# Kernel tuning notes

Hardware: AMD Instinct MI355X
Metric: run time of the kernel (lower is better)

Reference implementation:

```python
import jax, jax.numpy as jnp
import numpy as np

N = 4096; E = 32768; H = 128; R = 32; L = 2
CUT_UP = 5.0; MAX_Z = 100

def cosine_cutoff(d):
    c = 0.5 * (jnp.cos(d * (np.pi / CUT_UP)) + 1.0)
    return c * (d < CUT_UP).astype(d.dtype)

def tensor_norm(t):
    return (t * t).sum((-2, -1))

def decompose_tensor(t):
    eye = jnp.eye(3, dtype=t.dtype)
    I = (jnp.trace(t, axis1=-2, axis2=-1) / 3.0)[..., None, None] * eye
    tT = jnp.swapaxes(t, -2, -1)
    A = 0.5 * (t - tT)
    S = 0.5 * (t + tT) - I
    return I, A, S

def vector_to_skewtensor(v):
    x, y, z = v[..., 0], v[..., 1], v[..., 2]
    o = jnp.zeros_like(x)
    return jnp.stack([o, -z, y, z, o, -x, -y, x, o], axis=-1).reshape(v.shape[:-1] + (3, 3))

def vector_to_symtensor(v):
    t = v[..., :, None] * v[..., None, :]
    eye = jnp.eye(3, dtype=v.dtype)
    I = (jnp.trace(t, axis1=-2, axis2=-1) / 3.0)[..., None, None] * eye
    return t - I  # symmetric already, 0.5*(t+t^T) == t

def cmix(T, W):  # nn.Linear(H,H,bias=False) over the channel dim of [N,H,3,3]
    return jnp.einsum('nhij,hk->nkij', T, W)

def layernorm(x, g, b, eps=1e-5):
    m = x.mean(-1, keepdims=True)
    v = ((x - m) ** 2).mean(-1, keepdims=True)
    return (x - m) / jnp.sqrt(v + eps) * g + b

def setup_inputs():
    key = jax.random.key(0)
    ks = iter(jax.random.split(key, 48))
    def nrm(shape, fan_in):
        return jax.random.normal(next(ks), shape, jnp.float32) / np.sqrt(fan_in)
    inp = {}
    inp['z'] = jax.random.randint(next(ks), (N,), 0, MAX_Z)
    inp['edge_index'] = jax.random.randint(next(ks), (2, E), 0, N)
    inp['edge_weight'] = jax.random.uniform(next(ks), (E,), jnp.float32) * CUT_UP
    inp['edge_vec'] = jax.random.normal(next(ks), (E, 3), jnp.float32)
    inp['edge_attr'] = jax.random.normal(next(ks), (E, R), jnp.float32)
    inp['emb_table'] = nrm((MAX_Z, H), H)
    inp['dp1_w'] = nrm((R, H), R); inp['dp1_b'] = jnp.zeros((H,))
    inp['dp2_w'] = nrm((R, H), R); inp['dp2_b'] = jnp.zeros((H,))
    inp['dp3_w'] = nrm((R, H), R); inp['dp3_b'] = jnp.zeros((H,))
    inp['emb2_w'] = nrm((2 * H, H), 2 * H); inp['emb2_b'] = jnp.zeros((H,))
    inp['tne_lt'] = nrm((3, H, H), H)
    inp['tne_s0_w'] = nrm((H, 2 * H), H); inp['tne_s0_b'] = jnp.zeros((2 * H,))
    inp['tne_s1_w'] = nrm((2 * H, 3 * H), 2 * H); inp['tne_s1_b'] = jnp.zeros((3 * H,))
    inp['ln_g'] = jnp.ones((H,)); inp['ln_b'] = jnp.zeros((H,))
    inp['msg_l0_w'] = nrm((L, R, H), R); inp['msg_l0_b'] = jnp.zeros((L, H))
    inp['msg_l1_w'] = nrm((L, H, 2 * H), H); inp['msg_l1_b'] = jnp.zeros((L, 2 * H))
    inp['msg_l2_w'] = nrm((L, 2 * H, 3 * H), 2 * H); inp['msg_l2_b'] = jnp.zeros((L, 3 * H))
    inp['msg_lx'] = nrm((L, 3, H, H), H)
    inp['msg_lt'] = nrm((L, 3, H, H), H)
    return inp

def _forward(z, edge_index, edge_weight, edge_vec, edge_attr, emb_table,
             dp1_w, dp1_b, dp2_w, dp2_b, dp3_w, dp3_b, emb2_w, emb2_b,
             tne_lt, tne_s0_w, tne_s0_b, tne_s1_w, tne_s1_b, ln_g, ln_b,
             msg_l0_w, msg_l0_b, msg_l1_w, msg_l1_b, msg_l2_w, msg_l2_b,
             msg_lx, msg_lt):
    src, dst = edge_index[0], edge_index[1]
    eye = jnp.eye(3, dtype=jnp.float32)
    segsum = lambda x: jax.ops.segment_sum(x, dst, num_segments=N)
    silu = jax.nn.silu
    # ---- TensorNeighborEmbedding ----
    Z = emb_table[z]                                     # [N,H]
    C = cosine_cutoff(edge_weight)                       # [E]
    W1 = (edge_attr @ dp1_w + dp1_b) * C[:, None]
    W2 = (edge_attr @ dp2_w + dp2_b) * C[:, None]
    W3 = (edge_attr @ dp3_w + dp3_b) * C[:, None]
    mask = (src != dst)[:, None]
    vn = jnp.linalg.norm(edge_vec, axis=-1, keepdims=True)
    ev = jnp.where(mask, edge_vec / jnp.maximum(vn, 1e-12), edge_vec)
    skew = vector_to_skewtensor(ev)                      # [E,3,3]
    sym = vector_to_symtensor(ev)                        # [E,3,3]
    Zij = jnp.concatenate([Z[dst], Z[src]], axis=-1) @ emb2_w + emb2_b  # [E,H]
    # I channel is a scaled identity per edge -> factor the eye out of the scatter
    In = segsum(Zij * W1)[..., None, None] * eye                         # [N,H,3,3]
    An = segsum((Zij * W2)[:, :, None, None] * skew[:, None])            # [N,H,3,3]
    Sn = segsum((Zij * W3)[:, :, None, None] * sym[:, None])             # [N,H,3,3]
    norm = layernorm(tensor_norm(In + An + Sn), ln_g, ln_b)              # [N,H]
    In = cmix(In, tne_lt[0]); An = cmix(An, tne_lt[1]); Sn = cmix(Sn, tne_lt[2])
    fsc = silu(silu(norm @ tne_s0_w + tne_s0_b) @ tne_s1_w + tne_s1_b).reshape(N, H, 3)
    X = (fsc[..., 0, None, None] * In + fsc[..., 1, None, None] * An
         + fsc[..., 2, None, None] * Sn)
    # ---- TensorMessage layers ----
    for l in range(L):
        ea = silu(edge_attr @ msg_l0_w[l] + msg_l0_b[l])
        ea = silu(ea @ msg_l1_w[l] + msg_l1_b[l])
        ea = silu(ea @ msg_l2_w[l] + msg_l2_b[l])
        ea = (ea * C[:, None]).reshape(E, H, 3)
        X = X / (tensor_norm(X) + 1.0)[..., None, None]
        I, A, S = decompose_tensor(X)
        I = cmix(I, msg_lx[l, 0]); A = cmix(A, msg_lx[l, 1]); S = cmix(S, msg_lx[l, 2])
        Y = I + A + S
        Im = segsum(ea[:, :, 0, None, None] * I[src])    # gather -> scale -> scatter
        Am = segsum(ea[:, :, 1, None, None] * A[src])
        Sm = segsum(ea[:, :, 2, None, None] * S[src])
        msg = Im + Am + Sm
        AB = msg @ Y + Y @ msg                           # batched 3x3 matmuls
        I, A, S = decompose_tensor(AB)
        d = (tensor_norm(I + A + S) + 1.0)[..., None, None]
        I = cmix(I / d, msg_lt[l, 0]); A = cmix(A / d, msg_lt[l, 1]); S = cmix(S / d, msg_lt[l, 2])
        dX = I + A + S
        dX = dX + dX @ dX
        X = X + dX
    return X

def reference(z, edge_index, edge_weight, edge_vec, edge_attr, emb_table,
              dp1_w, dp1_b, dp2_w, dp2_b, dp3_w, dp3_b, emb2_w, emb2_b,
              tne_lt, tne_s0_w, tne_s0_b, tne_s1_w, tne_s1_b, ln_g, ln_b,
              msg_l0_w, msg_l0_b, msg_l1_w, msg_l1_b, msg_l2_w, msg_l2_b,
              msg_lx, msg_lt):
    return _forward(z, edge_index, edge_weight, edge_vec, edge_attr, emb_table,
                    dp1_w, dp1_b, dp2_w, dp2_b, dp3_w, dp3_b, emb2_w, emb2_b,
                    tne_lt, tne_s0_w, tne_s0_b, tne_s1_w, tne_s1_b, ln_g, ln_b,
                    msg_l0_w, msg_l0_b, msg_l1_w, msg_l1_b, msg_l2_w, msg_l2_b,
                    msg_lx, msg_lt)
```

## Files before the change

kernel.cpp:

```cpp
#include <hip/hip_runtime.h>
#include <hip/hip_bf16.h>

typedef __hip_bfloat16 bf16;
typedef __attribute__((ext_vector_type(8))) short short8v;
typedef __attribute__((ext_vector_type(4))) float f32x4;

#define NN 4096
#define NE 32768
#define HH 128
#define MAXZ 100
#define TPB 8
#define NB 2


__device__ __forceinline__ float b2f(bf16 v){ return __bfloat162float(v); }
__device__ __forceinline__ float ldf(const float* p, size_t i){ return p[i]; }
__device__ __forceinline__ float ldf(const bf16*  p, size_t i){ return __bfloat162float(p[i]); }
__device__ __forceinline__ float siluf(float x){ return x / (1.0f + __expf(-x)); }
__device__ __forceinline__ unsigned short f2bu(float x){
  bf16 h = __float2bfloat16(x);
  return *reinterpret_cast<unsigned short*>(&h);
}
__device__ __forceinline__ float bround(float x){
  bf16 h = __float2bfloat16(x);
  return __bfloat162float(h);
}

__global__ void __launch_bounds__(256) k_detect(const unsigned int* __restrict__ w, int* __restrict__ flag){
  __shared__ int cnt[256];
  int t = threadIdx.x;
  int c = 0;
  for (int i = t; i < 4096; i += 256){
    unsigned int lo = w[i] & 0xffffu;
    int e = (int)((lo >> 7) & 0xffu);
    c += (e >= 110 && e <= 132) ? 1 : 0;
  }
  cnt[t] = c; __syncthreads();
  for (int off=128; off>=1; off>>=1){ if (t<off) cnt[t]+=cnt[t+off]; __syncthreads(); }
  if (t==0) flag[0] = (cnt[0] < 2048) ? 1 : 0;
}

__global__ void __launch_bounds__(256) k_count(const int* __restrict__ dst, int* __restrict__ counts){
  int e = blockIdx.x*256 + threadIdx.x;
  if (e < NE) atomicAdd(&counts[dst[e]], 1);
}

__global__ void __launch_bounds__(1024) k_scan(const int* __restrict__ counts, int* __restrict__ offsets, int* __restrict__ cursor){
  __shared__ int lds[1024];
  int t = threadIdx.x;
  int c0 = counts[4*t+0], c1 = counts[4*t+1], c2 = counts[4*t+2], c3 = counts[4*t+3];
  int s1 = c0+c1, s2 = s1+c2, s3 = s2+c3;
  lds[t] = s3;
  __syncthreads();
  for (int off=1; off<1024; off<<=1){
    int v = lds[t];
    int add = (t>=off)? lds[t-off] : 0;
    __syncthreads();
    lds[t] = v + add;
    __syncthreads();
  }
  int incl = lds[t];
  int base = incl - s3;
  offsets[4*t+0]=base;    offsets[4*t+1]=base+c0; offsets[4*t+2]=base+s1; offsets[4*t+3]=base+s2;
  cursor [4*t+0]=base;    cursor [4*t+1]=base+c0; cursor [4*t+2]=base+s1; cursor [4*t+3]=base+s2;
  if (t==1023) offsets[4096]=incl;
}

__global__ void __launch_bounds__(256) k_fill(const int* __restrict__ dst, const int* __restrict__ src,
                                              int* __restrict__ cursor,
                                              int* __restrict__ pos, int* __restrict__ csrc){
  int e = blockIdx.x*256 + threadIdx.x;
  if (e < NE){
    int p = atomicAdd(&cursor[dst[e]], 1);
    pos[e] = p;
    csrc[p] = src[e];
  }
}

template<typename T>
__device__ __forceinline__ void geom_impl(const T* ew, const T* evec,
    const int* src, const int* dst, const int* pos, float* gC, float* gVp){
  int e = blockIdx.x*256 + threadIdx.x;
  if (e >= NE) return;
  float d = ldf(ew, e);
  float c = 0.5f*(cosf(d*0.6283185307179586f)+1.0f);
  c = (d < 5.0f) ? c : 0.0f;
  gC[e] = c;
  float x = ldf(evec, (size_t)e*3+0), y = ldf(evec, (size_t)e*3+1), z = ldf(evec, (size_t)e*3+2);
  if (src[e] != dst[e]){
    float n = sqrtf(x*x+y*y+z*z);
    float inv = 1.0f/fmaxf(n, 1e-12f);
    x*=inv; y*=inv; z*=inv;
  }
  int p = pos[e];
  gVp[p*3+0]=x; gVp[p*3+1]=y; gVp[p*3+2]=z;
}
__global__ void __launch_bounds__(256) k_geom(const void* ew, const void* evec,
    const int* __restrict__ src, const int* __restrict__ dst, const int* __restrict__ pos,
    float* __restrict__ gC, float* __restrict__ gVp, const int* __restrict__ flag){
  if (flag[0]) geom_impl<float>((const float*)ew, (const float*)evec, src, dst, pos, gC, gVp);
  else         geom_impl<bf16 >((const bf16* )ew, (const bf16* )evec, src, dst, pos, gC, gVp);
}

template<typename T>
__device__ __forceinline__ void zemb_impl(const T* emb, const T* emb2_w,
    float* P1z, float* P2z, float* Zr){
  int zv = blockIdx.x, h = threadIdx.x;
  Zr[h] = ldf(emb, (size_t)zv*HH + h);
  __syncthreads();
  float p1=0.f, p2=0.f;
  for (int r=0;r<128;++r){
    float x = Zr[r];
    p1 += x*ldf(emb2_w, (size_t)r*HH+h);
    p2 += x*ldf(emb2_w, (size_t)(r+128)*HH+h);
  }
  P1z[zv*HH+h]=p1; P2z[zv*HH+h]=p2;
}
__global__ void __launch_bounds__(128) k_zemb(const void* emb, const void* emb2_w,
    float* __restrict__ P1z, float* __restrict__ P2z, const int* __restrict__ flag){
  __shared__ float Zr[128];
  if (flag[0]) zemb_impl<float>((const float*)emb, (const float*)emb2_w, P1z, P2z, Zr);
  else         zemb_impl<bf16 >((const bf16* )emb, (const bf16* )emb2_w, P1z, P2z, Zr);
}

__global__ void __launch_bounds__(256) k_cvt_attr(const void* in, unsigned short* __restrict__ out,
                                                  const int* __restrict__ flag){
  int i = blockIdx.x*256 + threadIdx.x;
  if (flag[0]) out[i] = f2bu(((const float*)in)[i]);
  else         out[i] = ((const unsigned short*)in)[i];
}

struct PackDescs {
  const void*     base[23];
  long            eoff[23];
  unsigned short* out[23];
  int K[23]; int N[23];
};
template<typename T>
__device__ __forceinline__ void pack_impl(const PackDescs& d){
  int y = blockIdx.y;
  int K = d.K[y], N = d.N[y];
  int ktiles = K>>5, ntiles = N>>4;
  int total = ktiles*ntiles*64;
  int idx = blockIdx.x*256 + threadIdx.x;
  if (idx >= total) return;
  int lane = idx & 63, tile = idx >> 6;
  int kt = tile % ktiles, nt = tile / ktiles;
  const T* W = (const T*)d.base[y] + d.eoff[y];
  int n = nt*16 + (lane&15), k0 = kt*32 + (lane>>4)*8;
  unsigned int t[8];
  #pragma unroll
  for (int j=0;j<8;++j) t[j] = f2bu(ldf(W, (size_t)(k0+j)*N + n));
  uint4 v;
  v.x = t[0] | (t[1]<<16);
  v.y = t[2] | (t[3]<<16);
  v.z = t[4] | (t[5]<<16);
  v.w = t[6] | (t[7]<<16);
  *reinterpret_cast<uint4*>(d.out[y] + ((size_t)tile*64 + lane)*8) = v;
}
__global__ void __launch_bounds__(256) k_pack(PackDescs d, const int* __restrict__ flag){
  if (flag[0]) pack_impl<float>(d);
  else         pack_impl<bf16 >(d);
}

template<typename T>
__device__ __forceinline__ void tne_edge_impl(
  const T* eattr, const int* src, const int* dst, const int* z, const int* pos,
  const T* dp1_w, const T* dp1_b, const T* dp2_w, const T* dp2_b,
  const T* dp3_w, const T* dp3_b, const T* emb2_b,
  const float* P1z, const float* P2z, const float* gC, bf16* eabuf,
  float (*attr)[32], int* zd, int* zs, int* ppos)
{
  int e0 = blockIdx.x*TPB;
  int h  = threadIdx.x;
  for (int i=h; i<TPB*32; i+=128) attr[i>>5][i&31] = ldf(eattr, (size_t)e0*32 + i);
  if (h < TPB){ int e=e0+h; zd[h]=z[dst[e]]; zs[h]=z[src[e]]; ppos[h]=pos[e]; }
  __syncthreads();
  float w1[TPB], w2[TPB], w3[TPB];
  float b1v=ldf(dp1_b,h), b2v=ldf(dp2_b,h), b3v=ldf(dp3_b,h);
  #pragma unroll
  for (int e=0;e<TPB;++e){ w1[e]=b1v; w2[e]=b2v; w3[e]=b3v; }
  for (int r=0;r<32;++r){
    float u1=ldf(dp1_w,(size_t)r*HH+h), u2=ldf(dp2_w,(size_t)r*HH+h), u3=ldf(dp3_w,(size_t)r*HH+h);
    #pragma unroll
    for (int e=0;e<TPB;++e){ float a=attr[e][r]; w1[e]+=a*u1; w2[e]+=a*u2; w3[e]+=a*u3; }
  }
  float eb = ldf(emb2_b,h);
  #pragma unroll
  for (int e=0;e<TPB;++e){
    float zij = P1z[zd[e]*HH+h] + P2z[zs[e]*HH+h] + eb;
    float c = gC[e0+e];
    bf16* p = eabuf + (size_t)ppos[e]*384;
    p[h]     = __float2bfloat16(zij*w1[e]*c);
    p[128+h] = __float2bfloat16(zij*w2[e]*c);
    p[256+h] = __float2bfloat16(zij*w3[e]*c);
  }
}
__global__ void __launch_bounds__(128) k_tne_edge(
  const void* eattr, const int* __restrict__ src, const int* __restrict__ dst,
  const int* __restrict__ z, const int* __restrict__ pos,
  const void* dp1_w, const void* dp1_b, const void* dp2_w, const void* dp2_b,
  const void* dp3_w, const void* dp3_b, const void* emb2_b,
  const float* __restrict__ P1z, const float* __restrict__ P2z,
  const float* __restrict__ gC, bf16* __restrict__ eabuf, const int* __restrict__ flag)
{
  __shared__ float attr[TPB][32];
  __shared__ int zd[TPB], zs[TPB], ppos[TPB];
  if (flag[0]) tne_edge_impl<float>((const float*)eattr, src, dst, z, pos,
      (const float*)dp1_w, (const float*)dp1_b, (const float*)dp2_w, (const float*)dp2_b,
      (const float*)dp3_w, (const float*)dp3_b, (const float*)emb2_b, P1z, P2z, gC, eabuf, attr, zd, zs, ppos);
  else tne_edge_impl<bf16>((const bf16*)eattr, src, dst, z, pos,
      (const bf16*)dp1_w, (const bf16*)dp1_b, (const bf16*)dp2_w, (const bf16*)dp2_b,
      (const bf16*)dp3_w, (const bf16*)dp3_b, (const bf16*)emb2_b, P1z, P2z, gC, eabuf, attr, zd, zs, ppos);
}

template<typename T>
__device__ __forceinline__ void tne_scat_impl(
  const int* offsets, const float* gVp, const bf16* eabuf,
  const T* ln_g, const T* ln_b, bf16* sm10, bf16* lnO, float* red)
{
  int n0 = blockIdx.x*NB, h = threadIdx.x;
  float tnv[NB];
  #pragma unroll
  for (int nn=0;nn<NB;++nn){
    int n = n0+nn;
    float a=0, v0=0,v1=0,v2=0, s0=0,s1=0,s2=0,s3=0,s4=0,s5=0;
    int beg = offsets[n], end = offsets[n+1];
    int i = beg;
    for (; i+4 <= end; i += 4){
      float c1[4],c2[4],c3[4],vx[4],vy[4],vz[4];
      #pragma unroll
      for (int u=0;u<4;++u){
        const bf16* p = eabuf + (size_t)(i+u)*384;
        c1[u]=b2f(p[h]); c2[u]=b2f(p[128+h]); c3[u]=b2f(p[256+h]);
        vx[u]=gVp[(i+u)*3+0]; vy[u]=gVp[(i+u)*3+1]; vz[u]=gVp[(i+u)*3+2];
      }
      #pragma unroll
      for (int u=0;u<4;++u){
        float tr3 = (vx[u]*vx[u]+vy[u]*vy[u]+vz[u]*vz[u])*(1.0f/3.0f);
        a  += c1[u];
        v0 += c2[u]*vx[u]; v1 += c2[u]*vy[u]; v2 += c2[u]*vz[u];
        s0 += c3[u]*(vx[u]*vx[u] - tr3); s1 += c3[u]*vx[u]*vy[u]; s2 += c3[u]*vx[u]*vz[u];
        s3 += c3[u]*(vy[u]*vy[u] - tr3); s4 += c3[u]*vy[u]*vz[u]; s5 += c3[u]*(vz[u]*vz[u] - tr3);
      }
    }
    for (; i<end; ++i){
      const bf16* p = eabuf + (size_t)i*384;
      float c1 = b2f(p[h]), c2 = b2f(p[128+h]), c3 = b2f(p[256+h]);
      float vx = gVp[i*3+0], vy = gVp[i*3+1], vz = gVp[i*3+2];
      float tr3 = (vx*vx+vy*vy+vz*vz)*(1.0f/3.0f);
      a  += c1;
      v0 += c2*vx; v1 += c2*vy; v2 += c2*vz;
      s0 += c3*(vx*vx - tr3); s1 += c3*vx*vy;          s2 += c3*vx*vz;
      s3 += c3*(vy*vy - tr3); s4 += c3*vy*vz;          s5 += c3*(vz*vz - tr3);
    }
    bf16* sp = sm10 + (size_t)n*1280;
    sp[0*128+h]=__float2bfloat16(a);
    sp[1*128+h]=__float2bfloat16(v0); sp[2*128+h]=__float2bfloat16(v1); sp[3*128+h]=__float2bfloat16(v2);
    sp[4*128+h]=__float2bfloat16(s0); sp[5*128+h]=__float2bfloat16(s1); sp[6*128+h]=__float2bfloat16(s2);
    sp[7*128+h]=__float2bfloat16(s3); sp[8*128+h]=__float2bfloat16(s4); sp[9*128+h]=__float2bfloat16(s5);
    tnv[nn] = 3.0f*a*a + 2.0f*(v0*v0+v1*v1+v2*v2)
            + s0*s0 + s3*s3 + s5*s5 + 2.0f*(s1*s1 + s2*s2 + s4*s4);
  }
  float gg = ldf(ln_g,h), bb = ldf(ln_b,h);
  #pragma unroll
  for (int nn=0;nn<NB;++nn){
    __syncthreads();
    red[h] = tnv[nn]; __syncthreads();
    for (int off=64; off>=1; off>>=1){ if (h<off) red[h]+=red[h+off]; __syncthreads(); }
    float mean = red[0]*(1.0f/128.0f);
    __syncthreads();
    float dm = tnv[nn] - mean;
    red[h] = dm*dm; __syncthreads();
    for (int off=64; off>=1; off>>=1){ if (h<off) red[h]+=red[h+off]; __syncthreads(); }
    float var = red[0]*(1.0f/128.0f);
    lnO[(size_t)(n0+nn)*128 + h] = __float2bfloat16(dm*rsqrtf(var+1e-5f)*gg + bb);
  }
}
__global__ void __launch_bounds__(128) k_tne_scat(
  const int* __restrict__ offsets, const float* __restrict__ gVp, const bf16* __restrict__ eabuf,
  const void* ln_g, const void* ln_b, bf16* __restrict__ sm10, bf16* __restrict__ lnO,
  const int* __restrict__ flag)
{
  __shared__ float red[128];
  if (flag[0]) tne_scat_impl<float>(offsets, gVp, eabuf, (const float*)ln_g, (const float*)ln_b, sm10, lnO, red);
  else         tne_scat_impl<bf16 >(offsets, gVp, eabuf, (const bf16* )ln_g, (const bf16* )ln_b, sm10, lnO, red);
}

template<typename T>
__device__ __forceinline__ void node_mlp_impl(
  const bf16* lnO, const unsigned short* ps0, const unsigned short* ps1,
  const T* b0, const T* b1, bf16* fsc3, unsigned short* h2p)
{
  int wid  = threadIdx.x >> 6;
  int lane = threadIdx.x & 63;
  int n0 = blockIdx.x*16;
  int m = lane & 15, g = lane >> 4;
  short8v aln[4];
  #pragma unroll
  for (int ks=0; ks<4; ++ks)
    aln[ks] = *reinterpret_cast<const short8v*>((const unsigned short*)lnO + (size_t)(n0+m)*128 + ks*32 + g*8);
  for (int nt=wid; nt<16; nt+=4){
    float bias = ldf(b0, nt*16+m);
    f32x4 acc = {bias,bias,bias,bias};
    #pragma unroll
    for (int ks=0; ks<4; ++ks){
      short8v b = *reinterpret_cast<const short8v*>(ps0 + ((size_t)(nt*4+ks)*64 + lane)*8);
      acc = __builtin_amdgcn_mfma_f32_16x16x32_bf16(aln[ks], b, acc, 0,0,0);
    }
    #pragma unroll
    for (int r=0;r<4;++r){
      int n = nt*16 + m, row = g*4 + r;
      h2p[(n>>5)*512 + (((n>>3)&3)*16+row)*8 + (n&7)] = f2bu(siluf(acc[r]));
    }
  }
  __syncthreads();
  short8v a3[8];
  #pragma unroll
  for (int ks=0; ks<8; ++ks) a3[ks] = *reinterpret_cast<const short8v*>(&h2p[ks*512 + lane*8]);
  for (int nt=wid; nt<24; nt+=4){
    float bias = ldf(b1, nt*16+m);
    f32x4 acc = {bias,bias,bias,bias};
    #pragma unroll
    for (int ks=0; ks<8; ++ks){
      short8v b = *reinterpret_cast<const short8v*>(ps1 + ((size_t)(nt*8+ks)*64 + lane)*8);
      acc = __builtin_amdgcn_mfma_f32_16x16x32_bf16(a3[ks], b, acc, 0,0,0);
    }
    #pragma unroll
    for (int r=0;r<4;++r){
      int n = nt*16 + m, row = g*4 + r;
      ((unsigned short*)fsc3)[(size_t)(n0+row)*384 + (n%3)*128 + (n/3)] = f2bu(siluf(acc[r]));
    }
  }
}
__global__ void __launch_bounds__(256) k_node_mlp(
  const bf16* __restrict__ lnO, const unsigned short* __restrict__ ps0,
  const unsigned short* __restrict__ ps1,
  const void* b0, const void* b1, bf16* __restrict__ fsc3, const int* __restrict__ flag)
{
  __shared__ __align__(16) unsigned short h2p[4096];
  if (flag[0]) node_mlp_impl<float>(lnO, ps0, ps1, (const float*)b0, (const float*)b1, fsc3, h2p);
  else         node_mlp_impl<bf16 >(lnO, ps0, ps1, (const bf16* )b0, (const bf16* )b1, fsc3, h2p);
}

__global__ void __launch_bounds__(256) k_tne_cmix(
  const bf16* __restrict__ sm10, const unsigned short* __restrict__ pwlt,
  const bf16* __restrict__ fsc3, float* __restrict__ X9)
{
  int wid  = threadIdx.x >> 6;
  int lane = threadIdx.x & 63;
  int n0 = blockIdx.x*16;
  int m = lane & 15, g = lane >> 4;
  f32x4 acc[10][2];
  #pragma unroll
  for (int c=0;c<10;++c){ acc[c][0]=(f32x4){0,0,0,0}; acc[c][1]=(f32x4){0,0,0,0}; }
  #pragma unroll
  for (int c=0;c<10;++c){
    int mat = (c==0) ? 0 : (c<4) ? 1 : 2;
    const unsigned short* bw = pwlt + (size_t)mat*16384;
    short8v af[4];
    #pragma unroll
    for (int ks=0; ks<4; ++ks)
      af[ks] = *reinterpret_cast<const short8v*>((const unsigned short*)sm10 + (size_t)(n0+m)*1280 + c*128 + ks*32 + g*8);
    #pragma unroll
    for (int t=0;t<2;++t){
      int nt = wid + t*4;
      #pragma unroll
      for (int ks=0; ks<4; ++ks){
        short8v b = *reinterpret_cast<const short8v*>(bw + ((size_t)(nt*4+ks)*64 + lane)*8);
        acc[c][t] = __builtin_amdgcn_mfma_f32_16x16x32_bf16(af[ks], b, acc[c][t], 0,0,0);
      }
    }
  }
  #pragma unroll
  for (int t=0;t<2;++t){
    int nt = wid + t*4;
    int h = nt*16 + m;
    #pragma unroll
    for (int r=0;r<4;++r){
      int node = n0 + g*4 + r;
      float am  = acc[0][t][r];
      float wm0 = acc[1][t][r], wm1 = acc[2][t][r], wm2 = acc[3][t][r];
      float t0 = acc[4][t][r], t1 = acc[5][t][r], t2 = acc[6][t][r];
      float t3 = acc[7][t][r], t4 = acc[8][t][r], t5 = acc[9][t][r];
      float f0 = b2f(fsc3[(size_t)node*384 + h]);
      float f1 = b2f(fsc3[(size_t)node*384 + 128 + h]);
      float f2 = b2f(fsc3[(size_t)node*384 + 256 + h]);
      float* xp = X9 + (size_t)node*1152;
      xp[0*128+h] = f0*am + f2*t0;
      xp[1*128+h] = -f1*wm2 + f2*t1;
      xp[2*128+h] =  f1*wm1 + f2*t2;
      xp[3*128+h] =  f1*wm2 + f2*t1;
      xp[4*128+h] = f0*am + f2*t3;
      xp[5*128+h] = -f1*wm0 + f2*t4;
      xp[6*128+h] = -f1*wm1 + f2*t2;
      xp[7*128+h] =  f1*wm0 + f2*t4;
      xp[8*128+h] = f0*am + f2*t5;
    }
  }
}

__global__ void __launch_bounds__(256) k_cmix_norm(
  float* __restrict__ X9, const unsigned short* __restrict__ pw, bf16* __restrict__ Y10)
{
  __shared__ __align__(16) unsigned short sst[16*1280];
  int n0 = blockIdx.x*16;
  int tid = threadIdx.x;
  #pragma unroll
  for (int it=0; it<8; ++it){
    int idx = it*256 + tid;
    int nn = idx >> 7, h = idx & 127;
    float* xp = X9 + (size_t)(n0+nn)*1152;
    float x00=xp[0*128+h], x01=xp[1*128+h], x02=xp[2*128+h];
    float x10=xp[3*128+h], x11=xp[4*128+h], x12=xp[5*128+h];
    float x20=xp[6*128+h], x21=xp[7*128+h], x22=xp[8*128+h];
    float tn = x00*x00+x01*x01+x02*x02+x10*x10+x11*x11+x12*x12+x20*x20+x21*x21+x22*x22;
    float inv = 1.0f/(tn+1.0f);
    x00*=inv; x01*=inv; x02*=inv; x10*=inv; x11*=inv; x12*=inv; x20*=inv; x21*=inv; x22*=inv;
    xp[0*128+h]=x00; xp[1*128+h]=x01; xp[2*128+h]=x02;
    xp[3*128+h]=x10; xp[4*128+h]=x11; xp[5*128+h]=x12;
    xp[6*128+h]=x20; xp[7*128+h]=x21; xp[8*128+h]=x22;
    float a = (x00+x11+x22)*(1.0f/3.0f);
    unsigned short* sp = sst + (size_t)nn*1280;
    sp[0*128+h]=f2bu(a);
    sp[1*128+h]=f2bu(0.5f*(x21-x12));
    sp[2*128+h]=f2bu(0.5f*(x02-x20));
    sp[3*128+h]=f2bu(0.5f*(x10-x01));
    sp[4*128+h]=f2bu(x00-a);
    sp[5*128+h]=f2bu(0.5f*(x01+x10));
    sp[6*128+h]=f2bu(0.5f*(x02+x20));
    sp[7*128+h]=f2bu(x11-a);
    sp[8*128+h]=f2bu(0.5f*(x12+x21));
    sp[9*128+h]=f2bu(x22-a);
  }
  __syncthreads();
  int wid  = tid >> 6;
  int lane = tid & 63;
  int m = lane & 15, g = lane >> 4;
  f32x4 acc[10][2];
  #pragma unroll
  for (int c=0;c<10;++c){ acc[c][0]=(f32x4){0,0,0,0}; acc[c][1]=(f32x4){0,0,0,0}; }
  #pragma unroll
  for (int c=0;c<10;++c){
    int mat = (c==0) ? 0 : (c<4) ? 1 : 2;
    const unsigned short* bw = pw + (size_t)mat*16384;
    short8v af[4];
    #pragma unroll
    for (int ks=0; ks<4; ++ks)
      af[ks] = *reinterpret_cast<const short8v*>(&sst[(size_t)m*1280 + c*128 + ks*32 + g*8]);
    #pragma unroll
    for (int t=0;t<2;++t){
      int nt = wid + t*4;
      #pragma unroll
      for (int ks=0; ks<4; ++ks){
        short8v b = *reinterpret_cast<const short8v*>(bw + ((size_t)(nt*4+ks)*64 + lane)*8);
        acc[c][t] = __builtin_amdgcn_mfma_f32_16x16x32_bf16(af[ks], b, acc[c][t], 0,0,0);
      }
    }
  }
  #pragma unroll
  for (int t=0;t<2;++t){
    int nt = wid + t*4;
    int h = nt*16 + m;
    #pragma unroll
    for (int r=0;r<4;++r){
      int node = n0 + g*4 + r;
      unsigned short* op = (unsigned short*)Y10 + (size_t)node*1280;
      #pragma unroll
      for (int c=0;c<10;++c) op[c*128 + h] = f2bu(acc[c][t][r]);
    }
  }
}

template<typename T>
__device__ __forceinline__ void mfma_impl(
  const unsigned short* eattr_c, const float* gC, const int* pos,
  const unsigned short* p0, const unsigned short* p1, const unsigned short* p2,
  const T* b0, const T* b1, const T* b2,
  unsigned short* eabuf, unsigned short (*h1p)[2048], unsigned short (*h2p)[4096], int* spos)
{
  int wid  = threadIdx.x >> 6;
  int lane = threadIdx.x & 63;
  int e0 = blockIdx.x*32;
  int m = lane & 15, g = lane >> 4;
  if (threadIdx.x < 32) spos[threadIdx.x] = pos[e0 + threadIdx.x];
  float cc[2][4];
  #pragma unroll
  for (int mt=0;mt<2;++mt)
    #pragma unroll
    for (int r=0;r<4;++r) cc[mt][r] = gC[e0 + mt*16 + g*4 + r];
  short8v a1[2];
  #pragma unroll
  for (int mt=0;mt<2;++mt)
    a1[mt] = *reinterpret_cast<const short8v*>(eattr_c + (size_t)(e0+mt*16+m)*32 + g*8);
  for (int nt=wid; nt<8; nt+=4){
    float bias = ldf(b0, nt*16+m);
    short8v b = *reinterpret_cast<const short8v*>(p0 + ((size_t)nt*64 + lane)*8);
    #pragma unroll
    for (int mt=0;mt<2;++mt){
      f32x4 acc = {bias,bias,bias,bias};
      acc = __builtin_amdgcn_mfma_f32_16x16x32_bf16(a1[mt], b, acc, 0,0,0);
      #pragma unroll
      for (int r=0;r<4;++r){
        int n = nt*16 + m, row = g*4 + r;
        h1p[mt][(n>>5)*512 + (((n>>3)&3)*16+row)*8 + (n&7)] = f2bu(siluf(acc[r]));
      }
    }
  }
  __syncthreads();
  short8v a2[2][4];
  #pragma unroll
  for (int mt=0;mt<2;++mt)
    #pragma unroll
    for (int ks=0; ks<4; ++ks)
      a2[mt][ks] = *reinterpret_cast<const short8v*>(&h1p[mt][ks*512 + lane*8]);
  for (int nt=wid; nt<16; nt+=4){
    float bias = ldf(b1, nt*16+m);
    short8v bfr[4];
    #pragma unroll
    for (int ks=0; ks<4; ++ks)
      bfr[ks] = *reinterpret_cast<const short8v*>(p1 + ((size_t)(nt*4+ks)*64 + lane)*8);
    #pragma unroll
    for (int mt=0;mt<2;++mt){
      f32x4 acc = {bias,bias,bias,bias};
      #pragma unroll
      for (int ks=0; ks<4; ++ks)
        acc = __builtin_amdgcn_mfma_f32_16x16x32_bf16(a2[mt][ks], bfr[ks], acc, 0,0,0);
      #pragma unroll
      for (int r=0;r<4;++r){
        int n = nt*16 + m, row = g*4 + r;
        h2p[mt][(n>>5)*512 + (((n>>3)&3)*16+row)*8 + (n&7)] = f2bu(siluf(acc[r]));
      }
    }
  }
  __syncthreads();
  short8v a3[2][8];
  #pragma unroll
  for (int mt=0;mt<2;++mt)
    #pragma unroll
    for (int ks=0; ks<8; ++ks)
      a3[mt][ks] = *reinterpret_cast<const short8v*>(&h2p[mt][ks*512 + lane*8]);
  for (int nt=wid; nt<24; nt+=4){
    float bias = ldf(b2, nt*16+m);
    short8v bfr[8];
    #pragma unroll
    for (int ks=0; ks<8; ++ks)
      bfr[ks] = *reinterpret_cast<const short8v*>(p2 + ((size_t)(nt*8+ks)*64 + lane)*8);
    #pragma unroll
    for (int mt=0;mt<2;++mt){
      f32x4 acc = {bias,bias,bias,bias};
      #pragma unroll
      for (int ks=0; ks<8; ++ks)
        acc = __builtin_amdgcn_mfma_f32_16x16x32_bf16(a3[mt][ks], bfr[ks], acc, 0,0,0);
      #pragma unroll
      for (int r=0;r<4;++r){
        int n = nt*16 + m, row = g*4 + r;
        float v = siluf(acc[r]) * cc[mt][r];
        eabuf[(size_t)spos[mt*16+row]*384 + (n%3)*128 + (n/3)] = f2bu(v);
      }
    }
  }
}
__global__ void __launch_bounds__(256) k_msg_edge_mfma(
  const unsigned short* __restrict__ eattr_c, const float* __restrict__ gC,
  const int* __restrict__ pos,
  const unsigned short* __restrict__ p0a, const unsigned short* __restrict__ p0b,
  const unsigned short* __restrict__ p1a, const unsigned short* __restrict__ p1b,
  const unsigned short* __restrict__ p2a, const unsigned short* __restrict__ p2b,
  const void* b0, const void* b1, const void* b2,
  unsigned short* __restrict__ eabuf_msg, const int* __restrict__ flag)
{
  __shared__ __align__(16) unsigned short h1p[2][2048];
  __shared__ __align__(16) unsigned short h2p[2][4096];
  __shared__ int spos[32];
  int l = blockIdx.y;
  const unsigned short* p0 = l ? p0b : p0a;
  const unsigned short* p1 = l ? p1b : p1a;
  const unsigned short* p2 = l ? p2b : p2a;
  unsigned short* eabuf = eabuf_msg + (size_t)l*NE*384;
  if (flag[0]) mfma_impl<float>(eattr_c, gC, pos, p0, p1, p2,
      (const float*)b0 + (long)l*128, (const float*)b1 + (long)l*256, (const float*)b2 + (long)l*384,
      eabuf, h1p, h2p, spos);
  else mfma_impl<bf16>(eattr_c, gC, pos, p0, p1, p2,
      (const bf16*)b0 + (long)l*128, (const bf16*)b1 + (long)l*256, (const bf16*)b2 + (long)l*384,
      eabuf, h1p, h2p, spos);
}

__global__ void __launch_bounds__(128) k_msg_sab(
  const int* __restrict__ offsets, const int* __restrict__ csrc,
  const bf16* __restrict__ eabuf, const bf16* __restrict__ Y10, bf16* __restrict__ smb)
{
  int n0 = blockIdx.x*NB, h = threadIdx.x;
  #pragma unroll
  for (int nn=0;nn<NB;++nn){
    int n = n0+nn;
    float am=0, vm0=0,vm1=0,vm2=0, smm0=0,smm1=0,smm2=0,smm3=0,smm4=0,smm5=0;
    int beg = offsets[n], end = offsets[n+1];
    int i = beg;
    for (; i+4 <= end; i += 4){
      int ss[4];
      #pragma unroll
      for (int u=0;u<4;++u){ ss[u] = csrc[i+u]; }
      float e0a[4], e1a[4], e2a[4];
      float y0[4],y1[4],y2[4],y3[4],y4[4],y5[4],y6[4],y7[4],y8[4],y9[4];
      #pragma unroll
      for (int u=0;u<4;++u){
        const bf16* ep = eabuf + (size_t)(i+u)*384;
        e0a[u]=b2f(ep[h]); e1a[u]=b2f(ep[128+h]); e2a[u]=b2f(ep[256+h]);
        const bf16* yp = Y10 + (size_t)ss[u]*1280;
        y0[u]=b2f(yp[0*128+h]); y1[u]=b2f(yp[1*128+h]); y2[u]=b2f(yp[2*128+h]);
        y3[u]=b2f(yp[3*128+h]); y4[u]=b2f(yp[4*128+h]); y5[u]=b2f(yp[5*128+h]);
        y6[u]=b2f(yp[6*128+h]); y7[u]=b2f(yp[7*128+h]); y8[u]=b2f(yp[8*128+h]);
        y9[u]=b2f(yp[9*128+h]);
      }
      #pragma unroll
      for (int u=0;u<4;++u){
        am   += e0a[u]*y0[u];
        vm0  += e1a[u]*y1[u]; vm1 += e1a[u]*y2[u]; vm2 += e1a[u]*y3[u];
        smm0 += e2a[u]*y4[u]; smm1 += e2a[u]*y5[u]; smm2 += e2a[u]*y6[u];
        smm3 += e2a[u]*y7[u]; smm4 += e2a[u]*y8[u]; smm5 += e2a[u]*y9[u];
      }
    }
    for (; i<end; ++i){
      int s = csrc[i];
      const bf16* ep = eabuf + (size_t)i*384;
      float e0 = b2f(ep[h]), e1 = b2f(ep[128+h]), e2 = b2f(ep[256+h]);
      const bf16* yp = Y10 + (size_t)s*1280;
      am   += e0*b2f(yp[0*128+h]);
      vm0  += e1*b2f(yp[1*128+h]); vm1 += e1*b2f(yp[2*128+h]); vm2 += e1*b2f(yp[3*128+h]);
      smm0 += e2*b2f(yp[4*128+h]); smm1 += e2*b2f(yp[5*128+h]); smm2 += e2*b2f(yp[6*128+h]);
      smm3 += e2*b2f(yp[7*128+h]); smm4 += e2*b2f(yp[8*128+h]); smm5 += e2*b2f(yp[9*128+h]);
    }
    const bf16* yp = Y10 + (size_t)n*1280;
    float aY=b2f(yp[0*128+h]), u0=b2f(yp[1*128+h]), u1=b2f(yp[2*128+h]), u2=b2f(yp[3*128+h]);
    float q0=b2f(yp[4*128+h]), q1=b2f(yp[5*128+h]), q2=b2f(yp[6*128+h]);
    float q3=b2f(yp[7*128+h]), q4=b2f(yp[8*128+h]), q5=b2f(yp[9*128+h]);
    float m00=am+smm0,   m01=-vm2+smm1, m02= vm1+smm2;
    float m10= vm2+smm1, m11=am+smm3,  m12=-vm0+smm4;
    float m20=-vm1+smm2, m21= vm0+smm4, m22=am+smm5;
    float y00=aY+q0,  y01=-u2+q1, y02= u1+q2;
    float y10= u2+q1, y11=aY+q3,  y12=-u0+q4;
    float y20=-u1+q2, y21= u0+q4, y22=aY+q5;
    float ab00 = m00*y00+m01*y10+m02*y20 + y00*m00+y01*m10+y02*m20;
    float ab01 = m00*y01+m01*y11+m02*y21 + y00*m01+y01*m11+y02*m21;
    float ab02 = m00*y02+m01*y12+m02*y22 + y00*m02+y01*m12+y02*m22;
    float ab10 = m10*y00+m11*y10+m12*y20 + y10*m00+y11*m10+y12*m20;
    float ab11 = m10*y01+m11*y11+m12*y21 + y10*m01+y11*m11+y12*m21;
    float ab12 = m10*y02+m11*y12+m12*y22 + y10*m02+y11*m12+y12*m22;
    float ab20 = m20*y00+m21*y10+m22*y20 + y20*m00+y21*m10+y22*m20;
    float ab21 = m20*y01+m21*y11+m22*y21 + y20*m01+y21*m11+y22*m21;
    float ab22 = m20*y02+m21*y12+m22*y22 + y20*m02+y21*m12+y22*m22;
    float a2 = (ab00+ab11+ab22)*(1.0f/3.0f);
    float w0 = 0.5f*(ab21-ab12), w1 = 0.5f*(ab02-ab20), w2 = 0.5f*(ab10-ab01);
    float t0 = ab00-a2, t1 = 0.5f*(ab01+ab10), t2 = 0.5f*(ab02+ab20);
    float t3 = ab11-a2, t4 = 0.5f*(ab12+ab21), t5 = ab22-a2;
    float dnm = ab00*ab00+ab01*ab01+ab02*ab02+ab10*ab10+ab11*ab11+ab12*ab12
              + ab20*ab20+ab21*ab21+ab22*ab22 + 1.0f;
    float inv = 1.0f/dnm;
    bf16* sp = smb + (size_t)n*1280;
    sp[0*128+h]=__float2bfloat16(a2*inv);
    sp[1*128+h]=__float2bfloat16(w0*inv); sp[2*128+h]=__float2bfloat16(w1*inv); sp[3*128+h]=__float2bfloat16(w2*inv);
    sp[4*128+h]=__float2bfloat16(t0*inv); sp[5*128+h]=__float2bfloat16(t1*inv); sp[6*128+h]=__float2bfloat16(t2*inv);
    sp[7*128+h]=__float2bfloat16(t3*inv); sp[8*128+h]=__float2bfloat16(t4*inv); sp[9*128+h]=__float2bfloat16(t5*inv);
  }
}

template<typename T>
__device__ __forceinline__ void cmix_fin_impl(
  const bf16* smb, const unsigned short* pw, float* X9, T* out, int write_out)
{
  int wid  = threadIdx.x >> 6;
  int lane = threadIdx.x & 63;
  int n0 = blockIdx.x*16;
  int m = lane & 15, g = lane >> 4;
  f32x4 acc[10][2];
  #pragma unroll
  for (int c=0;c<10;++c){ acc[c][0]=(f32x4){0,0,0,0}; acc[c][1]=(f32x4){0,0,0,0}; }
  #pragma unroll
  for (int c=0;c<10;++c){
    int mat = (c==0) ? 0 : (c<4) ? 1 : 2;
    const unsigned short* bw = pw + (size_t)mat*16384;
    short8v af[4];
    #pragma unroll
    for (int ks=0; ks<4; ++ks)
      af[ks] = *reinterpret_cast<const short8v*>((const unsigned short*)smb + (size_t)(n0+m)*1280 + c*128 + ks*32 + g*8);
    #pragma unroll
    for (int t=0;t<2;++t){
      int nt = wid + t*4;
      #pragma unroll
      for (int ks=0; ks<4; ++ks){
        short8v b = *reinterpret_cast<const short8v*>(bw + ((size_t)(nt*4+ks)*64 + lane)*8);
        acc[c][t] = __builtin_amdgcn_mfma_f32_16x16x32_bf16(af[ks], b, acc[c][t], 0,0,0);
      }
    }
  }
  #pragma unroll
  for (int t=0;t<2;++t){
    int nt = wid + t*4;
    int h = nt*16 + m;
    #pragma unroll
    for (int r=0;r<4;++r){
      int node = n0 + g*4 + r;
      float at  = bround(acc[0][t][r]);
      float vt0 = bround(acc[1][t][r]), vt1 = bround(acc[2][t][r]), vt2 = bround(acc[3][t][r]);
      float st0 = bround(acc[4][t][r]), st1 = bround(acc[5][t][r]), st2 = bround(acc[6][t][r]);
      float st3 = bround(acc[7][t][r]), st4 = bround(acc[8][t][r]), st5 = bround(acc[9][t][r]);
      float d00=at+st0,   d01=-vt2+st1, d02= vt1+st2;
      float d10= vt2+st1, d11=at+st3,  d12=-vt0+st4;
      float d20=-vt1+st2, d21= vt0+st4, d22=at+st5;
      float g00 = d00 + d00*d00+d01*d10+d02*d20;
      float g01 = d01 + d00*d01+d01*d11+d02*d21;
      float g02 = d02 + d00*d02+d01*d12+d02*d22;
      float g10 = d10 + d10*d00+d11*d10+d12*d20;
      float g11 = d11 + d10*d01+d11*d11+d12*d21;
      float g12 = d12 + d10*d02+d11*d12+d12*d22;
      float g20 = d20 + d20*d00+d21*d10+d22*d20;
      float g21 = d21 + d20*d01+d21*d11+d22*d21;
      float g22 = d22 + d20*d02+d21*d12+d22*d22;
      float* xp = X9 + (size_t)node*1152;
      float x00=xp[0*128+h]+g00, x01=xp[1*128+h]+g01, x02=xp[2*128+h]+g02;
      float x10=xp[3*128+h]+g10, x11=xp[4*128+h]+g11, x12=xp[5*128+h]+g12;
      float x20=xp[6*128+h]+g20, x21=xp[7*128+h]+g21, x22=xp[8*128+h]+g22;
      if (write_out){
        if (sizeof(T)==4){
          float* of = (float*)out + ((size_t)node*128 + h)*9;
          of[0]=x00; of[1]=x01; of[2]=x02; of[3]=x10; of[4]=x11; of[5]=x12; of[6]=x20; of[7]=x21; of[8]=x22;
        } else {
          bf16* ob = (bf16*)out + ((size_t)node*128 + h)*9;
          ob[0]=__float2bfloat16(x00); ob[1]=__float2bfloat16(x01); ob[2]=__float2bfloat16(x02);
          ob[3]=__float2bfloat16(x10); ob[4]=__float2bfloat16(x11); ob[5]=__float2bfloat16(x12);
          ob[6]=__float2bfloat16(x20); ob[7]=__float2bfloat16(x21); ob[8]=__float2bfloat16(x22);
        }
      } else {
        xp[0*128+h]=x00; xp[1*128+h]=x01; xp[2*128+h]=x02;
        xp[3*128+h]=x10; xp[4*128+h]=x11; xp[5*128+h]=x12;
        xp[6*128+h]=x20; xp[7*128+h]=x21; xp[8*128+h]=x22;
      }
    }
  }
}
__global__ void __launch_bounds__(256) k_cmix_fin(
  const bf16* __restrict__ smb, const unsigned short* __restrict__ pw,
  float* __restrict__ X9, void* __restrict__ out,
  const int* __restrict__ flag, int write_out)
{
  if (flag[0]) cmix_fin_impl<float>(smb, pw, X9, (float*)out, write_out);
  else         cmix_fin_impl<bf16 >(smb, pw, X9, (bf16* )out, write_out);
}

extern "C" void kernel_launch(void* const* d_in, const int* in_sizes, int n_in,
                              void* d_out, int out_size, void* d_ws, size_t ws_size,
                              hipStream_t stream)
{
  (void)in_sizes; (void)n_in; (void)out_size; (void)ws_size;
  const int* z    = (const int*)d_in[0];
  const int* eidx = (const int*)d_in[1];
  const int* src  = eidx;
  const int* dst  = eidx + NE;

  char* w = (char*)d_ws;
  int* flag    = (int*)w;   w += 64;
  int* counts  = (int*)w;   w += (size_t)NN*4;
  int* offsets = (int*)w;   w += (size_t)(NN+1)*4 + 60;
  int* cursor  = (int*)w;   w += (size_t)NN*4;
  int* pos     = (int*)w;   w += (size_t)NE*4;
  int* csrc    = (int*)w;   w += (size_t)NE*4;
  float* gC    = (float*)w; w += (size_t)NE*4;
  float* gVp   = (float*)w; w += (size_t)NE*12;
  float* P1z   = (float*)w; w += (size_t)MAXZ*HH*4;
  float* P2z   = (float*)w; w += (size_t)MAXZ*HH*4;
  bf16* eabuf  = (bf16*)w;  w += (size_t)NE*384*2;
  bf16* eabuf_msg = (bf16*)w; w += (size_t)2*NE*384*2;
  float* X9    = (float*)w; w += (size_t)NN*1152*4;
  bf16* Y10    = (bf16*)w;  w += (size_t)NN*1280*2;
  bf16* smb    = (bf16*)w;  w += (size_t)NN*1280*2;
  unsigned short* eattr_c = (unsigned short*)w; w += (size_t)NE*32*2;
  unsigned short* pw0[2]; unsigned short* pw1[2]; unsigned short* pw2[2];
  for (int l=0;l<2;++l){
    pw0[l] = (unsigned short*)w; w += 8*64*8*2;
    pw1[l] = (unsigned short*)w; w += 64*64*8*2;
    pw2[l] = (unsigned short*)w; w += 192*64*8*2;
  }
  unsigned short* pw_s0 = (unsigned short*)w; w += 64*64*8*2;
  unsigned short* pw_s1 = (unsigned short*)w; w += 192*64*8*2;
  unsigned short* pwlt  = (unsigned short*)w; w += 3*32*64*8*2;
  unsigned short* pwlx2 = (unsigned short*)w; w += 2*3*32*64*8*2;
  unsigned short* pwlt2 = (unsigned short*)w; w += 2*3*32*64*8*2;
  bf16* lnO    = (bf16*)w;  w += (size_t)NN*128*2;
  bf16* fsc3   = (bf16*)w;  w += (size_t)NN*384*2;
  bf16* sm10   = Y10;

  k_detect<<<1, 256, 0, stream>>>((const unsigned int*)d_in[4], flag);
  hipMemsetAsync(counts, 0, (size_t)NN*4, stream);
  k_count<<<NE/256, 256, 0, stream>>>(dst, counts);
  k_scan<<<1, 1024, 0, stream>>>(counts, offsets, cursor);
  k_fill<<<NE/256, 256, 0, stream>>>(dst, src, cursor, pos, csrc);
  k_geom<<<NE/256, 256, 0, stream>>>(d_in[2], d_in[3], src, dst, pos, gC, gVp, flag);
  k_zemb<<<MAXZ, 128, 0, stream>>>(d_in[5], d_in[12], P1z, P2z, flag);
  k_cvt_attr<<<NE*32/256, 256, 0, stream>>>(d_in[4], eattr_c, flag);

  PackDescs pd;
  for (int l=0;l<2;++l){
    pd.base[l*3+0] = d_in[21]; pd.eoff[l*3+0] = (long)l*32*128;
    pd.base[l*3+1] = d_in[23]; pd.eoff[l*3+1] = (long)l*128*256;
    pd.base[l*3+2] = d_in[25]; pd.eoff[l*3+2] = (long)l*256*384;
    pd.out[l*3+0] = pw0[l]; pd.K[l*3+0]=32;  pd.N[l*3+0]=128;
    pd.out[l*3+1] = pw1[l]; pd.K[l*3+1]=128; pd.N[l*3+1]=256;
    pd.out[l*3+2] = pw2[l]; pd.K[l*3+2]=256; pd.N[l*3+2]=384;
  }
  pd.base[6] = d_in[15]; pd.eoff[6] = 0; pd.out[6] = pw_s0; pd.K[6]=128; pd.N[6]=256;
  pd.base[7] = d_in[17]; pd.eoff[7] = 0; pd.out[7] = pw_s1; pd.K[7]=256; pd.N[7]=384;
  for (int c=0;c<3;++c){
    pd.base[8+c] = d_in[14]; pd.eoff[8+c] = (long)c*16384;
    pd.out[8+c] = pwlt + (size_t)c*16384; pd.K[8+c]=128; pd.N[8+c]=128;
  }
  for (int l=0;l<2;++l)
    for (int c=0;c<3;++c){
      pd.base[11+l*3+c] = d_in[27]; pd.eoff[11+l*3+c] = (long)(l*3+c)*16384;
      pd.out[11+l*3+c] = pwlx2 + (size_t)(l*3+c)*16384; pd.K[11+l*3+c]=128; pd.N[11+l*3+c]=128;
      pd.base[17+l*3+c] = d_in[28]; pd.eoff[17+l*3+c] = (long)(l*3+c)*16384;
      pd.out[17+l*3+c] = pwlt2 + (size_t)(l*3+c)*16384; pd.K[17+l*3+c]=128; pd.N[17+l*3+c]=128;
    }
  k_pack<<<dim3(48, 23), 256, 0, stream>>>(pd, flag);

  k_msg_edge_mfma<<<dim3(NE/32, 2), 256, 0, stream>>>(eattr_c, gC, pos,
      pw0[0], pw0[1], pw1[0], pw1[1], pw2[0], pw2[1],
      d_in[22], d_in[24], d_in[26],
      (unsigned short*)eabuf_msg, flag);

  k_tne_edge<<<NE/TPB, 128, 0, stream>>>(d_in[4], src, dst, z, pos,
      d_in[6], d_in[7], d_in[8], d_in[9], d_in[10], d_in[11], d_in[13],
      P1z, P2z, gC, eabuf, flag);
  k_tne_scat<<<NN/NB, 128, 0, stream>>>(offsets, gVp, eabuf,
      d_in[19], d_in[20], sm10, lnO, flag);
  k_node_mlp<<<NN/16, 256, 0, stream>>>(lnO, pw_s0, pw_s1, d_in[16], d_in[18], fsc3, flag);
  k_tne_cmix<<<NN/16, 256, 0, stream>>>(sm10, pwlt, fsc3, X9);

  for (int l=0; l<2; ++l){
    k_cmix_norm<<<NN/16, 256, 0, stream>>>(X9, pwlx2 + (size_t)l*3*16384, Y10);
    k_msg_sab<<<NN/NB, 128, 0, stream>>>(offsets, csrc,
        eabuf_msg + (size_t)l*NE*384, Y10, smb);
    k_cmix_fin<<<NN/16, 256, 0, stream>>>(smb, pwlt2 + (size_t)l*3*16384, X9, d_out,
        flag, (l==1)?1:0);
  }
}
```

Before: 250.3 us.

## Stage edge MLP output in LDS for coalesced scatter, halve edges per block

The per-edge message MLP kernel now handles 16 edges per block instead of 32, which doubles the grid and cuts LDS and register use per block. The final layer's outputs are no longer scattered element by element to global memory. They are staged in a padded shared buffer and written out as 16-byte rows per edge, giving coalesced writes to the permuted edge position. The trade-off is that each weight fragment is loaded once per 16 edges rather than 32, doubling weight traffic, and there are extra barriers.

```diff
diff --git a/kernel.cpp b/kernel.cpp
--- a/kernel.cpp
+++ b/kernel.cpp
@@ -477,88 +477,76 @@
   const unsigned short* eattr_c, const float* gC, const int* pos,
   const unsigned short* p0, const unsigned short* p1, const unsigned short* p2,
   const T* b0, const T* b1, const T* b2,
-  unsigned short* eabuf, unsigned short (*h1p)[2048], unsigned short (*h2p)[4096], int* spos)
+  unsigned short* eabuf, unsigned short* buf, int* spos)
 {
   int wid  = threadIdx.x >> 6;
   int lane = threadIdx.x & 63;
-  int e0 = blockIdx.x*32;
+  int e0 = blockIdx.x*16;
   int m = lane & 15, g = lane >> 4;
-  if (threadIdx.x < 32) spos[threadIdx.x] = pos[e0 + threadIdx.x];
-  float cc[2][4];
-  #pragma unroll
-  for (int mt=0;mt<2;++mt)
-    #pragma unroll
-    for (int r=0;r<4;++r) cc[mt][r] = gC[e0 + mt*16 + g*4 + r];
-  short8v a1[2];
-  #pragma unroll
-  for (int mt=0;mt<2;++mt)
-    a1[mt] = *reinterpret_cast<const short8v*>(eattr_c + (size_t)(e0+mt*16+m)*32 + g*8);
+  if (threadIdx.x < 16) spos[threadIdx.x] = pos[e0 + threadIdx.x];
+  float cc[4];
+  #pragma unroll
+  for (int r=0;r<4;++r) cc[r] = gC[e0 + g*4 + r];
+  unsigned short* h1p = buf;
+  unsigned short* h2p = buf + 2048;
+  short8v a1 = *reinterpret_cast<const short8v*>(eattr_c + (size_t)(e0+m)*32 + g*8);
   for (int nt=wid; nt<8; nt+=4){
     float bias = ldf(b0, nt*16+m);
+    f32x4 acc = {bias,bias,bias,bias};
     short8v b = *reinterpret_cast<const short8v*>(p0 + ((size_t)nt*64 + lane)*8);
-    #pragma unroll
-    for (int mt=0;mt<2;++mt){
-      f32x4 acc = {bias,bias,bias,bias};
-      acc = __builtin_amdgcn_mfma_f32_16x16x32_bf16(a1[mt], b, acc, 0,0,0);
-      #pragma unroll
-      for (int r=0;r<4;++r){
-        int n = nt*16 + m, row = g*4 + r;
-        h1p[mt][(n>>5)*512 + (((n>>3)&3)*16+row)*8 + (n&7)] = f2bu(siluf(acc[r]));
-      }
+    acc = __builtin_amdgcn_mfma_f32_16x16x32_bf16(a1, b, acc, 0,0,0);
+    #pragma unroll
+    for (int r=0;r<4;++r){
+      int n = nt*16 + m, row = g*4 + r;
+      h1p[(n>>5)*512 + (((n>>3)&3)*16+row)*8 + (n&7)] = f2bu(siluf(acc[r]));
     }
   }
   __syncthreads();
-  short8v a2[2][4];
-  #pragma unroll
-  for (int mt=0;mt<2;++mt)
-    #pragma unroll
-    for (int ks=0; ks<4; ++ks)
-      a2[mt][ks] = *reinterpret_cast<const short8v*>(&h1p[mt][ks*512 + lane*8]);
+  short8v a2[4];
+  #pragma unroll
+  for (int ks=0; ks<4; ++ks) a2[ks] = *reinterpret_cast<const short8v*>(&h1p[ks*512 + lane*8]);
   for (int nt=wid; nt<16; nt+=4){
     float bias = ldf(b1, nt*16+m);
-    short8v bfr[4];
-    #pragma unroll
-    for (int ks=0; ks<4; ++ks)
-      bfr[ks] = *reinterpret_cast<const short8v*>(p1 + ((size_t)(nt*4+ks)*64 + lane)*8);
-    #pragma unroll
-    for (int mt=0;mt<2;++mt){
-      f32x4 acc = {bias,bias,bias,bias};
-      #pragma unroll
-      for (int ks=0; ks<4; ++ks)
-        acc = __builtin_amdgcn_mfma_f32_16x16x32_bf16(a2[mt][ks], bfr[ks], acc, 0,0,0);
-      #pragma unroll
-      for (int r=0;r<4;++r){
-        int n = nt*16 + m, row = g*4 + r;
-        h2p[mt][(n>>5)*512 + (((n>>3)&3)*16+row)*8 + (n&7)] = f2bu(siluf(acc[r]));
-      }
+    f32x4 acc = {bias,bias,bias,bias};
+    #pragma unroll
+    for (int ks=0; ks<4; ++ks){
+      short8v b = *reinterpret_cast<const short8v*>(p1 + ((size_t)(nt*4+ks)*64 + lane)*8);
+      acc = __builtin_amdgcn_mfma_f32_16x16x32_bf16(a2[ks], b, acc, 0,0,0);
+    }
+    #pragma unroll
+    for (int r=0;r<4;++r){
+      int n = nt*16 + m, row = g*4 + r;
+      h2p[(n>>5)*512 + (((n>>3)&3)*16+row)*8 + (n&7)] = f2bu(siluf(acc[r]));
     }
   }
   __syncthreads();
-  short8v a3[2][8];
-  #pragma unroll
-  for (int mt=0;mt<2;++mt)
-    #pragma unroll
-    for (int ks=0; ks<8; ++ks)
-      a3[mt][ks] = *reinterpret_cast<const short8v*>(&h2p[mt][ks*512 + lane*8]);
+  short8v a3[8];
+  #pragma unroll
+  for (int ks=0; ks<8; ++ks) a3[ks] = *reinterpret_cast<const short8v*>(&h2p[ks*512 + lane*8]);
+  __syncthreads();
   for (int nt=wid; nt<24; nt+=4){
     float bias = ldf(b2, nt*16+m);
-    short8v bfr[8];
-    #pragma unroll
-    for (int ks=0; ks<8; ++ks)
-      bfr[ks] = *reinterpret_cast<const short8v*>(p2 + ((size_t)(nt*8+ks)*64 + lane)*8);
-    #pragma unroll
-    for (int mt=0;mt<2;++mt){
-      f32x4 acc = {bias,bias,bias,bias};
-      #pragma unroll
-      for (int ks=0; ks<8; ++ks)
-        acc = __builtin_amdgcn_mfma_f32_16x16x32_bf16(a3[mt][ks], bfr[ks], acc, 0,0,0);
-      #pragma unroll
-      for (int r=0;r<4;++r){
-        int n = nt*16 + m, row = g*4 + r;
-        float v = siluf(acc[r]) * cc[mt][r];
-        eabuf[(size_t)spos[mt*16+row]*384 + (n%3)*128 + (n/3)] = f2bu(v);
-      }
-    }
+    f32x4 acc = {bias,bias,bias,bias};
+    #pragma unroll
+    for (int ks=0; ks<8; ++ks){
+      short8v b = *reinterpret_cast<const short8v*>(p2 + ((size_t)(nt*8+ks)*64 + lane)*8);
+      acc = __builtin_amdgcn_mfma_f32_16x16x32_bf16(a3[ks], b, acc, 0,0,0);
+    }
+    #pragma unroll
+    for (int r=0;r<4;++r){
+      int n = nt*16 + m, row = g*4 + r;
+      float v = siluf(acc[r]) * cc[r];
+      buf[row*392 + (n%3)*128 + (n/3)] = f2bu(v);
+    }
+  }
+  __syncthreads();
+  int r  = threadIdx.x >> 4;
+  int ch = threadIdx.x & 15;
+  size_t base = (size_t)spos[r]*384;
+  #pragma unroll
+  for (int it=0; it<3; ++it){
+    uint4 v = *reinterpret_cast<const uint4*>(&buf[r*392 + (ch + it*16)*8]);
+    *reinterpret_cast<uint4*>(eabuf + base + (size_t)(ch + it*16)*8) = v;
   }
 }
 __global__ void __launch_bounds__(256) k_msg_edge_mfma(
@@ -570,9 +558,8 @@
   const void* b0, const void* b1, const void* b2,
   unsigned short* __restrict__ eabuf_msg, const int* __restrict__ flag)
 {
-  __shared__ __align__(16) unsigned short h1p[2][2048];
-  __shared__ __align__(16) unsigned short h2p[2][4096];
-  __shared__ int spos[32];
+  __shared__ __align__(16) unsigned short buf[6272];
+  __shared__ int spos[16];
   int l = blockIdx.y;
   const unsigned short* p0 = l ? p0b : p0a;
   const unsigned short* p1 = l ? p1b : p1a;
@@ -580,10 +567,10 @@
   unsigned short* eabuf = eabuf_msg + (size_t)l*NE*384;
   if (flag[0]) mfma_impl<float>(eattr_c, gC, pos, p0, p1, p2,
       (const float*)b0 + (long)l*128, (const float*)b1 + (long)l*256, (const float*)b2 + (long)l*384,
-      eabuf, h1p, h2p, spos);
+      eabuf, buf, spos);
   else mfma_impl<bf16>(eattr_c, gC, pos, p0, p1, p2,
       (const bf16*)b0 + (long)l*128, (const bf16*)b1 + (long)l*256, (const bf16*)b2 + (long)l*384,
-      eabuf, h1p, h2p, spos);
+      eabuf, buf, spos);
 }
 
 __global__ void __launch_bounds__(128) k_msg_sab(
@@ -823,7 +810,7 @@
     }
   k_pack<<<dim3(48, 23), 256, 0, stream>>>(pd, flag);
 
-  k_msg_edge_mfma<<<dim3(NE/32, 2), 256, 0, stream>>>(eattr_c, gC, pos,
+  k_msg_edge_mfma<<<dim3(NE/16, 2), 256, 0, stream>>>(eattr_c, gC, pos,
       pw0[0], pw0[1], pw1[0], pw1[1], pw2[0], pw2[1],
       d_in[22], d_in[24], d_in[26],
       (unsigned short*)eabuf_msg, flag);
```

Result: faster. 234.0 us (-6.5%).
